# Kernel optimization log

Hardware: AMD Instinct MI355X
Metric: run time of the kernel (lower is better)

Reference implementation:

```python
import jax, jax.numpy as jnp
import numpy as np

N, C, H, W = 512, 256, 14, 14
EPS = 1e-5


def _conv(x, w, pad):
    # x: [N,C,H,W], w: [O,I,kh,kw]
    return jax.lax.conv_general_dilated(
        x, w, window_strides=(1, 1), padding=[(pad, pad), (pad, pad)],
        dimension_numbers=("NCHW", "OIHW", "NCHW"))


def setup_inputs() -> dict:
    key = jax.random.key(0)
    ks = jax.random.split(key, 12)
    x = jax.random.normal(ks[0], (N, C, H, W), jnp.float32)
    gc = jax.random.normal(ks[1], (N, C, H, W), jnp.float32)
    # valid boxes: xmin,ymin in [0,800), w,h in [20,170)
    xy = jax.random.uniform(ks[2], (N, 2), jnp.float32) * 800.0
    wh = jax.random.uniform(ks[3], (N, 2), jnp.float32) * 150.0 + 20.0
    boxes = jnp.concatenate([xy, xy + wh], axis=1)
    classes = jax.random.randint(ks[4], (N,), 0, 2, jnp.int32)
    s3 = 1.0 / np.sqrt(C * 9)
    s1 = 1.0 / np.sqrt(C)
    Wc3 = jax.random.normal(ks[5], (C, C, 3, 3), jnp.float32) * s3
    Wc1 = jax.random.normal(ks[6], (C, C, 1, 1), jnp.float32) * s1
    Wt3 = jax.random.normal(ks[7], (C, C, 3, 3), jnp.float32) * s3
    Wt1 = jax.random.normal(ks[8], (C, C, 1, 1), jnp.float32) * s1
    Wf3 = jax.random.normal(ks[9], (C, C, 3, 3), jnp.float32) * s3
    Wf1 = jax.random.normal(ks[10], (C, C, 1, 1), jnp.float32) * s1
    bn_gamma = jnp.ones((C,), jnp.float32)
    bn_beta = jnp.zeros((C,), jnp.float32)
    bn_mean = jnp.zeros((C,), jnp.float32)
    bn_var = jnp.ones((C,), jnp.float32)
    return dict(x=x, global_context=gc, boxes=boxes, classes=classes,
                Wc3=Wc3, Wc1=Wc1, Wt3=Wt3, Wt1=Wt1, Wf3=Wf3, Wf1=Wf1,
                bn_gamma=bn_gamma, bn_beta=bn_beta, bn_mean=bn_mean, bn_var=bn_var)


def reference(x, global_context, boxes, classes, Wc3, Wc1, Wt3, Wt1, Wf3, Wf1,
              bn_gamma, bn_beta, bn_mean, bn_var):
    # pairwise intersection / self-area gating
    area = (boxes[:, 2] - boxes[:, 0]) * (boxes[:, 3] - boxes[:, 1])  # [N]
    lt = jnp.maximum(boxes[:, None, :2], boxes[None, :, :2])  # [N,N,2]
    rb = jnp.minimum(boxes[:, None, 2:], boxes[None, :, 2:])
    wh = jnp.clip(rb - lt, 0.0)
    inter = wh[..., 0] * wh[..., 1]                            # [N,N]
    inter_percent = inter / area[None, :]                      # divide by area of box j
    mask = (inter_percent > 0.9).astype(x.dtype)               # [N,N]; diag always 1
    counts = mask.sum(axis=1)                                  # [N] >= 1
    # per-instance gather-average of member features
    avg = jnp.einsum("ij,jchw->ichw", mask, x) / counts[:, None, None, None]
    text_in = jnp.where((counts > 1.0)[:, None, None, None], avg, x)
    # branch convs (batched instead of per-proposal loop)
    char_out = _conv(_conv(x, Wc3, 1), Wc1, 0)
    text_out = _conv(_conv(text_in, Wt3, 1), Wt1, 0)
    char_context = jnp.where((classes != 0)[:, None, None, None], char_out, text_out)
    fuse = char_context + x + global_context
    y = _conv(_conv(fuse, Wf3, 1), Wf1, 0)
    inv = jax.lax.rsqrt(bn_var + EPS)
    y = (y - bn_mean[None, :, None, None]) * (bn_gamma * inv)[None, :, None, None] \
        + bn_beta[None, :, None, None]
    return jax.nn.relu(y)
```

## Files before the change

kernel.cpp:

```cpp
#include <hip/hip_runtime.h>

typedef unsigned short u16;
typedef unsigned int u32;
typedef __bf16 bf16x8 __attribute__((ext_vector_type(8)));
typedef float f32x4 __attribute__((ext_vector_type(4)));
typedef u16 u16x4 __attribute__((ext_vector_type(4)));
typedef float f4v __attribute__((ext_vector_type(4)));

#define NB   512
#define CCH  256
#define HW   196
#define LROW 40
#define SSTR 53248

__device__ inline u16 f2bf(float f) {
    u32 u = __float_as_uint(f);
    u32 r = (u + 0x7FFFu + ((u >> 16) & 1u)) >> 16;
    return (u16)r;
}

__global__ void wconv_kernel(const float* __restrict__ Wc3, const float* __restrict__ Wt3,
                             const float* __restrict__ Wf3, const float* __restrict__ Wc1,
                             const float* __restrict__ Wt1, const float* __restrict__ Wf1,
                             u16* __restrict__ w3, u16* __restrict__ w1o)
{
    int bid = blockIdx.x, tid = threadIdx.x;
    if (bid < 768) {
        int wsel = bid >> 8;
        int co = bid & 255;
        const float* src = wsel == 0 ? Wc3 : (wsel == 1 ? Wt3 : Wf3);
#pragma unroll
        for (int rs = 0; rs < 9; ++rs) {
            float v = src[(co * 256 + tid) * 9 + rs];
            w3[wsel * 589824 + (rs * 256 + co) * 256 + tid] = f2bf(v);
        }
    } else {
        int k = (bid - 768) * 256 + tid;
        int wsel = k >> 14;
        int rem = k & 16383;
        const float* src = wsel == 0 ? Wc1 : (wsel == 1 ? Wt1 : Wf1);
        f4v v = *(const f4v*)(src + rem * 4);
        u16x4 o = { f2bf(v.x), f2bf(v.y), f2bf(v.z), f2bf(v.w) };
        *(u16x4*)(w1o + wsel * 65536 + rem * 4) = o;
    }
}

__global__ void mask_kernel(const float* __restrict__ boxes, int* __restrict__ counts,
                            int* __restrict__ members)
{
    int i = blockIdx.x;
    int ln = threadIdx.x;
    __shared__ int cnt;
    if (ln == 0) cnt = 0;
    __syncthreads();
    float xi0 = boxes[i * 4 + 0], yi0 = boxes[i * 4 + 1];
    float xi1 = boxes[i * 4 + 2], yi1 = boxes[i * 4 + 3];
    for (int j = ln; j < NB; j += 64) {
        float xj0 = boxes[j * 4 + 0], yj0 = boxes[j * 4 + 1];
        float xj1 = boxes[j * 4 + 2], yj1 = boxes[j * 4 + 3];
        float areaj = (xj1 - xj0) * (yj1 - yj0);
        float lx = fmaxf(xi0, xj0), ly = fmaxf(yi0, yj0);
        float rx = fminf(xi1, xj1), ry = fminf(yi1, yj1);
        float w = fmaxf(rx - lx, 0.f), h = fmaxf(ry - ly, 0.f);
        if (w * h / areaj > 0.9f) {
            int p = atomicAdd(&cnt, 1);
            members[i * NB + p] = j;
        }
    }
    __syncthreads();
    if (ln == 0) counts[i] = cnt;
}

__global__ void bin_kernel(const float* __restrict__ x, const int* __restrict__ classes,
                           const int* __restrict__ counts, const int* __restrict__ members,
                           u16* __restrict__ bin)
{
    const int s = blockIdx.x, tid = threadIdx.x;
    const int cnt = counts[s];
    u16* binS = bin + s * SSTR;
    if (classes[s] != 0 || cnt <= 1) {
        for (int v = tid; v < 64 * 208; v += 256) {
            int c4 = v / 208;
            int px = v - c4 * 208;
            u16x4 o = {0, 0, 0, 0};
            if (px < HW) {
#pragma unroll
                for (int rg = 0; rg < 4; ++rg)
                    o[rg] = f2bf(x[(s * CCH + c4 * 4 + rg) * HW + px]);
            }
            *(u16x4*)(binS + (c4 * 208 + px) * 4) = o;
        }
    } else {
        __shared__ int mem[NB];
        for (int u = tid; u < cnt; u += 256) mem[u] = members[s * NB + u];
        __syncthreads();
        const float inv = 1.f / (float)cnt;
        for (int v = tid; v < 64 * 208; v += 256) {
            int c4 = v / 208;
            int px = v - c4 * 208;
            u16x4 o = {0, 0, 0, 0};
            if (px < HW) {
                float a[4] = {0.f, 0.f, 0.f, 0.f};
                for (int k = 0; k < cnt; ++k) {
                    const float* xm = x + mem[k] * (CCH * HW);
#pragma unroll
                    for (int rg = 0; rg < 4; ++rg)
                        a[rg] += xm[(c4 * 4 + rg) * HW + px];
                }
#pragma unroll
                for (int rg = 0; rg < 4; ++rg) o[rg] = f2bf(a[rg] * inv);
            }
            *(u16x4*)(binS + (c4 * 208 + px) * 4) = o;
        }
    }
}

__global__ __launch_bounds__(256, 2) void conv3x3_kernel(
    const u16* __restrict__ in, u16* __restrict__ out,
    const u16* __restrict__ w0, const u16* __restrict__ w1,
    const int* __restrict__ classes, int useClass)
{
    __shared__ u16 lds[197 * LROW];
    const int tid = threadIdx.x;
    const int bid = blockIdx.x;
    const int s = bid >> 1;
    const int th = bid & 1;
    const int wv = tid >> 6;
    const int ln = tid & 63;
    const int q = ln >> 4;
    const int l15 = ln & 15;
    const int cobase = wv * 64;
    const int t0 = th * 7;
    const int NT = th ? 6 : 7;

    const u16* wsel = (useClass && classes[s] == 0) ? w1 : w0;

    if (tid < 20) ((u32*)lds)[196 * (LROW / 2) + tid] = 0u;

    int baddr[7], vbits[7];
#pragma unroll
    for (int t = 0; t < 7; ++t) {
        int tt = t0 + t;
        int px = tt * 16 + l15;
        int vb = 0;
        int ba = 196 * LROW + q * 8;
        if (t < NT && px < HW) {
            int y = px / 14;
            int x = px - y * 14;
            ba = px * LROW + q * 8;
#pragma unroll
            for (int rs = 0; rs < 9; ++rs) {
                int iy = y + rs / 3 - 1;
                int ix = x + rs % 3 - 1;
                if (iy >= 0 && iy < 14 && ix >= 0 && ix < 14) vb |= 1 << rs;
            }
        }
        baddr[t] = ba;
        vbits[t] = vb;
    }

    f32x4 acc[4][7];
#pragma unroll
    for (int a = 0; a < 4; ++a)
#pragma unroll
        for (int t = 0; t < 7; ++t) acc[a][t] = (f32x4){0.f, 0.f, 0.f, 0.f};

    const u16* inS = in + s * SSTR;

    for (int cc = 0; cc < 8; ++cc) {
        __syncthreads();
        for (int v = tid; v < 1568; v += 256) {
            int ci4 = v & 7;
            int px = v >> 3;
            u16x4 val = *(const u16x4*)(inS + ((cc * 8 + ci4) * 208 + px) * 4);
            *(u16x4*)(lds + px * LROW + ci4 * 4) = val;
        }
        __syncthreads();

#pragma unroll
        for (int rs = 0; rs < 9; ++rs) {
            const int d = (rs / 3 - 1) * 14 + (rs % 3 - 1);
            bf16x8 af[4];
#pragma unroll
            for (int sub = 0; sub < 4; ++sub)
                af[sub] = *(const bf16x8*)(wsel + ((rs * 256 + cobase + sub * 16 + l15) * 256 + cc * 32 + q * 8));
#pragma unroll
            for (int t = 0; t < 7; ++t) {
                if (t < NT) {
                    int addr = ((vbits[t] >> rs) & 1) ? (baddr[t] + d * LROW)
                                                      : (196 * LROW + q * 8);
                    bf16x8 b = *(const bf16x8*)(lds + addr);
#pragma unroll
                    for (int sub = 0; sub < 4; ++sub)
                        acc[sub][t] = __builtin_amdgcn_mfma_f32_16x16x32_bf16(af[sub], b, acc[sub][t], 0, 0, 0);
                }
            }
        }
    }

#pragma unroll
    for (int sub = 0; sub < 4; ++sub) {
        int co4 = (cobase >> 2) + sub * 4 + q;
#pragma unroll
        for (int t = 0; t < 7; ++t) {
            if (t < NT) {
                int pxs = (t0 + t) * 16 + l15;
                u16x4 o = { f2bf(acc[sub][t][0]), f2bf(acc[sub][t][1]),
                            f2bf(acc[sub][t][2]), f2bf(acc[sub][t][3]) };
                *(u16x4*)(out + (s * (size_t)SSTR) + (co4 * 208 + pxs) * 4) = o;
            }
        }
    }
}

template <int MODE>
__global__ __launch_bounds__(256, 2) void conv1x1_kernel(
    const u16* __restrict__ in, const u16* __restrict__ w0, const u16* __restrict__ w1,
    const int* __restrict__ classes, int useClass,
    const float* __restrict__ xin, const float* __restrict__ gcin,
    const float* __restrict__ gamma, const float* __restrict__ beta,
    const float* __restrict__ mean, const float* __restrict__ var,
    void* __restrict__ outv)
{
    __shared__ u16 lds[197 * LROW];
    const int tid = threadIdx.x;
    const int bid = blockIdx.x;
    const int s = bid >> 1;
    const int th = bid & 1;
    const int wv = tid >> 6;
    const int ln = tid & 63;
    const int q = ln >> 4;
    const int l15 = ln & 15;
    const int cobase = wv * 64;
    const int t0 = th * 7;
    const int NT = th ? 6 : 7;

    const u16* wsel = (useClass && classes[s] == 0) ? w1 : w0;

    if (tid < 20) ((u32*)lds)[196 * (LROW / 2) + tid] = 0u;

    int baddr[7];
#pragma unroll
    for (int t = 0; t < 7; ++t) {
        int px = (t0 + t) * 16 + l15;
        baddr[t] = (t < NT && px < HW ? px : 196) * LROW + q * 8;
    }

    f32x4 acc[4][7];
#pragma unroll
    for (int a = 0; a < 4; ++a)
#pragma unroll
        for (int t = 0; t < 7; ++t) acc[a][t] = (f32x4){0.f, 0.f, 0.f, 0.f};

    const u16* inS = in + s * SSTR;

    for (int cc = 0; cc < 8; ++cc) {
        __syncthreads();
        for (int v = tid; v < 1568; v += 256) {
            int ci4 = v & 7;
            int px = v >> 3;
            u16x4 val = *(const u16x4*)(inS + ((cc * 8 + ci4) * 208 + px) * 4);
            *(u16x4*)(lds + px * LROW + ci4 * 4) = val;
        }
        __syncthreads();

        bf16x8 af[4];
#pragma unroll
        for (int sub = 0; sub < 4; ++sub)
            af[sub] = *(const bf16x8*)(wsel + ((cobase + sub * 16 + l15) * 256 + cc * 32 + q * 8));
#pragma unroll
        for (int t = 0; t < 7; ++t) {
            if (t < NT) {
                bf16x8 b = *(const bf16x8*)(lds + baddr[t]);
#pragma unroll
                for (int sub = 0; sub < 4; ++sub)
                    acc[sub][t] = __builtin_amdgcn_mfma_f32_16x16x32_bf16(af[sub], b, acc[sub][t], 0, 0, 0);
            }
        }
    }

    if (MODE == 0) {
        u16* outb = (u16*)outv;
#pragma unroll
        for (int sub = 0; sub < 4; ++sub) {
            int co4 = (cobase >> 2) + sub * 4 + q;
#pragma unroll
            for (int t = 0; t < 7; ++t) {
                if (t < NT) {
                    int pxs = (t0 + t) * 16 + l15;
                    u16x4 o = {0, 0, 0, 0};
                    if (pxs < HW) {
#pragma unroll
                        for (int rg = 0; rg < 4; ++rg) {
                            int idx = (s * CCH + co4 * 4 + rg) * HW + pxs;
                            o[rg] = f2bf(acc[sub][t][rg] + xin[idx] + gcin[idx]);
                        }
                    }
                    *(u16x4*)(outb + (s * (size_t)SSTR) + (co4 * 208 + pxs) * 4) = o;
                }
            }
        }
    } else {
        float* outf = (float*)outv;
        float scl[4][4], mn[4][4], bt[4][4];
#pragma unroll
        for (int sub = 0; sub < 4; ++sub)
#pragma unroll
            for (int rg = 0; rg < 4; ++rg) {
                int c = cobase + sub * 16 + q * 4 + rg;
                scl[sub][rg] = gamma[c] * rsqrtf(var[c] + 1e-5f);
                mn[sub][rg] = mean[c];
                bt[sub][rg] = beta[c];
            }
#pragma unroll
        for (int sub = 0; sub < 4; ++sub)
#pragma unroll
            for (int t = 0; t < 7; ++t) {
                if (t < NT) {
                    int pxs = (t0 + t) * 16 + l15;
                    if (pxs < HW) {
#pragma unroll
                        for (int rg = 0; rg < 4; ++rg) {
                            int co = cobase + sub * 16 + q * 4 + rg;
                            float v = (acc[sub][t][rg] - mn[sub][rg]) * scl[sub][rg] + bt[sub][rg];
                            outf[(s * CCH + co) * HW + pxs] = fmaxf(v, 0.f);
                        }
                    }
                }
            }
    }
}

extern "C" void kernel_launch(void* const* d_in, const int* in_sizes, int n_in,
                              void* d_out, int out_size, void* d_ws, size_t ws_size,
                              hipStream_t stream)
{
    const float* x    = (const float*)d_in[0];
    const float* gc   = (const float*)d_in[1];
    const float* boxes= (const float*)d_in[2];
    const int*   cls  = (const int*)d_in[3];
    const float* Wc3  = (const float*)d_in[4];
    const float* Wc1  = (const float*)d_in[5];
    const float* Wt3  = (const float*)d_in[6];
    const float* Wt1  = (const float*)d_in[7];
    const float* Wf3  = (const float*)d_in[8];
    const float* Wf1  = (const float*)d_in[9];
    const float* gam  = (const float*)d_in[10];
    const float* bet  = (const float*)d_in[11];
    const float* mea  = (const float*)d_in[12];
    const float* var  = (const float*)d_in[13];
    float* out = (float*)d_out;
    char* ws = (char*)d_ws;

    u16* w3      = (u16*)(ws);
    u16* w1o     = (u16*)(ws + 3538944);
    int* counts  = (int*)(ws + 3932160);
    int* members = (int*)(ws + 3934208);
    u16* bufA    = (u16*)(ws + 4982784);
    u16* bufB    = (u16*)(ws + 59508736);

    wconv_kernel<<<960, 256, 0, stream>>>(Wc3, Wt3, Wf3, Wc1, Wt1, Wf1, w3, w1o);
    mask_kernel<<<512, 64, 0, stream>>>(boxes, counts, members);
    bin_kernel<<<512, 256, 0, stream>>>(x, cls, counts, members, bufA);
    conv3x3_kernel<<<1024, 256, 0, stream>>>(bufA, bufB, w3, w3 + 589824, cls, 1);
    conv1x1_kernel<0><<<1024, 256, 0, stream>>>(bufB, w1o, w1o + 65536, cls, 1, x, gc,
                                                nullptr, nullptr, nullptr, nullptr, (void*)bufA);
    conv3x3_kernel<<<1024, 256, 0, stream>>>(bufA, bufB, w3 + 2 * 589824, w3, cls, 0);
    conv1x1_kernel<1><<<1024, 256, 0, stream>>>(bufB, w1o + 2 * 65536, w1o, cls, 0, nullptr, nullptr,
                                                gam, bet, mea, var, (void*)out);
}
```

Measured before the change: 910.1 us.

## Retile convs by output-channel group and stage 3x3 weights in LDS

Each block now handles one sample and one 64-channel output group instead of half the pixels with all channels. The four waves split the pixel tiles between them and share a single weight slice. For the 3x3 conv, the weights are re-laid out per channel group and chunk, then staged cooperatively into LDS so that all waves reuse them rather than each loading A fragments from global memory. In exchange the activation tile is reloaded four times per sample, LDS use per block grows, and occupancy is raised to 3 blocks per SM.

Result: faster. 872.4 us (-4.1%).

```diff
diff --git a/kernel.cpp b/kernel.cpp
--- a/kernel.cpp
+++ b/kernel.cpp
@@ -5,13 +5,17 @@
 typedef __bf16 bf16x8 __attribute__((ext_vector_type(8)));
 typedef float f32x4 __attribute__((ext_vector_type(4)));
 typedef u16 u16x4 __attribute__((ext_vector_type(4)));
+typedef u16 u16x8 __attribute__((ext_vector_type(8)));
 typedef float f4v __attribute__((ext_vector_type(4)));
 
 #define NB   512
 #define CCH  256
 #define HW   196
 #define LROW 40
+#define ACT_ELEMS (197 * LROW)
+#define WLDS_ELEMS (9 * 64 * 32)
 #define SSTR 53248
+#define CGSTR 147456
 
 __device__ inline u16 f2bf(float f) {
     u32 u = __float_as_uint(f);
@@ -26,13 +30,15 @@
 {
     int bid = blockIdx.x, tid = threadIdx.x;
     if (bid < 768) {
-        int wsel = bid >> 8;
+        int wset = bid >> 8;
         int co = bid & 255;
-        const float* src = wsel == 0 ? Wc3 : (wsel == 1 ? Wt3 : Wf3);
+        int cgi = co >> 6, cop = co & 63;
+        int cc = tid >> 5, cip = tid & 31;
+        const float* src = wset == 0 ? Wc3 : (wset == 1 ? Wt3 : Wf3);
 #pragma unroll
         for (int rs = 0; rs < 9; ++rs) {
             float v = src[(co * 256 + tid) * 9 + rs];
-            w3[wsel * 589824 + (rs * 256 + co) * 256 + tid] = f2bf(v);
+            w3[wset * 589824 + cgi * CGSTR + (cc * 9 + rs) * 2048 + cop * 32 + cip] = f2bf(v);
         }
     } else {
         int k = (bid - 768) * 256 + tid;
@@ -115,33 +121,31 @@
     }
 }
 
-__global__ __launch_bounds__(256, 2) void conv3x3_kernel(
+__global__ __launch_bounds__(256, 3) void conv3x3_kernel(
     const u16* __restrict__ in, u16* __restrict__ out,
     const u16* __restrict__ w0, const u16* __restrict__ w1,
     const int* __restrict__ classes, int useClass)
 {
-    __shared__ u16 lds[197 * LROW];
+    __shared__ u16 lds[ACT_ELEMS + WLDS_ELEMS];
     const int tid = threadIdx.x;
     const int bid = blockIdx.x;
-    const int s = bid >> 1;
-    const int th = bid & 1;
+    const int s  = bid >> 2;
+    const int cg = bid & 3;
     const int wv = tid >> 6;
     const int ln = tid & 63;
     const int q = ln >> 4;
     const int l15 = ln & 15;
-    const int cobase = wv * 64;
-    const int t0 = th * 7;
-    const int NT = th ? 6 : 7;
-
-    const u16* wsel = (useClass && classes[s] == 0) ? w1 : w0;
+    const int t0 = (wv == 0) ? 0 : (wv == 1 ? 4 : (wv == 2 ? 7 : 10));
+    const int NT = (wv == 0) ? 4 : 3;
+
+    const u16* wsel = (((useClass && classes[s] == 0) ? w1 : w0)) + cg * CGSTR;
 
     if (tid < 20) ((u32*)lds)[196 * (LROW / 2) + tid] = 0u;
 
-    int baddr[7], vbits[7];
-#pragma unroll
-    for (int t = 0; t < 7; ++t) {
-        int tt = t0 + t;
-        int px = tt * 16 + l15;
+    int baddr[4], vbits[4];
+#pragma unroll
+    for (int t = 0; t < 4; ++t) {
+        int px = (t0 + t) * 16 + l15;
         int vb = 0;
         int ba = 196 * LROW + q * 8;
         if (t < NT && px < HW) {
@@ -159,11 +163,11 @@
         vbits[t] = vb;
     }
 
-    f32x4 acc[4][7];
+    f32x4 acc[4][4];
 #pragma unroll
     for (int a = 0; a < 4; ++a)
 #pragma unroll
-        for (int t = 0; t < 7; ++t) acc[a][t] = (f32x4){0.f, 0.f, 0.f, 0.f};
+        for (int t = 0; t < 4; ++t) acc[a][t] = (f32x4){0.f, 0.f, 0.f, 0.f};
 
     const u16* inS = in + s * SSTR;
 
@@ -175,6 +179,14 @@
             u16x4 val = *(const u16x4*)(inS + ((cc * 8 + ci4) * 208 + px) * 4);
             *(u16x4*)(lds + px * LROW + ci4 * 4) = val;
         }
+        {
+            const u16* wcc = wsel + cc * WLDS_ELEMS;
+#pragma unroll
+            for (int k = 0; k < 9; ++k) {
+                int idx = tid + k * 256;
+                *(u16x8*)(lds + ACT_ELEMS + idx * 8) = *(const u16x8*)(wcc + idx * 8);
+            }
+        }
         __syncthreads();
 
 #pragma unroll
@@ -183,9 +195,9 @@
             bf16x8 af[4];
 #pragma unroll
             for (int sub = 0; sub < 4; ++sub)
-                af[sub] = *(const bf16x8*)(wsel + ((rs * 256 + cobase + sub * 16 + l15) * 256 + cc * 32 + q * 8));
-#pragma unroll
-            for (int t = 0; t < 7; ++t) {
+                af[sub] = *(const bf16x8*)(lds + ACT_ELEMS + rs * 2048 + (sub * 16 + l15) * 32 + q * 8);
+#pragma unroll
+            for (int t = 0; t < 4; ++t) {
                 if (t < NT) {
                     int addr = ((vbits[t] >> rs) & 1) ? (baddr[t] + d * LROW)
                                                       : (196 * LROW + q * 8);
@@ -200,9 +212,9 @@
 
 #pragma unroll
     for (int sub = 0; sub < 4; ++sub) {
-        int co4 = (cobase >> 2) + sub * 4 + q;
-#pragma unroll
-        for (int t = 0; t < 7; ++t) {
+        int co4 = cg * 16 + sub * 4 + q;
+#pragma unroll
+        for (int t = 0; t < 4; ++t) {
             if (t < NT) {
                 int pxs = (t0 + t) * 16 + l15;
                 u16x4 o = { f2bf(acc[sub][t][0]), f2bf(acc[sub][t][1]),
@@ -214,7 +226,7 @@
 }
 
 template <int MODE>
-__global__ __launch_bounds__(256, 2) void conv1x1_kernel(
+__global__ __launch_bounds__(256, 3) void conv1x1_kernel(
     const u16* __restrict__ in, const u16* __restrict__ w0, const u16* __restrict__ w1,
     const int* __restrict__ classes, int useClass,
     const float* __restrict__ xin, const float* __restrict__ gcin,
@@ -222,35 +234,34 @@
     const float* __restrict__ mean, const float* __restrict__ var,
     void* __restrict__ outv)
 {
-    __shared__ u16 lds[197 * LROW];
+    __shared__ u16 lds[ACT_ELEMS];
     const int tid = threadIdx.x;
     const int bid = blockIdx.x;
-    const int s = bid >> 1;
-    const int th = bid & 1;
+    const int s  = bid >> 2;
+    const int cg = bid & 3;
     const int wv = tid >> 6;
     const int ln = tid & 63;
     const int q = ln >> 4;
     const int l15 = ln & 15;
-    const int cobase = wv * 64;
-    const int t0 = th * 7;
-    const int NT = th ? 6 : 7;
+    const int t0 = (wv == 0) ? 0 : (wv == 1 ? 4 : (wv == 2 ? 7 : 10));
+    const int NT = (wv == 0) ? 4 : 3;
 
     const u16* wsel = (useClass && classes[s] == 0) ? w1 : w0;
 
     if (tid < 20) ((u32*)lds)[196 * (LROW / 2) + tid] = 0u;
 
-    int baddr[7];
-#pragma unroll
-    for (int t = 0; t < 7; ++t) {
+    int baddr[4];
+#pragma unroll
+    for (int t = 0; t < 4; ++t) {
         int px = (t0 + t) * 16 + l15;
         baddr[t] = (t < NT && px < HW ? px : 196) * LROW + q * 8;
     }
 
-    f32x4 acc[4][7];
+    f32x4 acc[4][4];
 #pragma unroll
     for (int a = 0; a < 4; ++a)
 #pragma unroll
-        for (int t = 0; t < 7; ++t) acc[a][t] = (f32x4){0.f, 0.f, 0.f, 0.f};
+        for (int t = 0; t < 4; ++t) acc[a][t] = (f32x4){0.f, 0.f, 0.f, 0.f};
 
     const u16* inS = in + s * SSTR;
 
@@ -267,9 +278,9 @@
         bf16x8 af[4];
 #pragma unroll
         for (int sub = 0; sub < 4; ++sub)
-            af[sub] = *(const bf16x8*)(wsel + ((cobase + sub * 16 + l15) * 256 + cc * 32 + q * 8));
-#pragma unroll
-        for (int t = 0; t < 7; ++t) {
+            af[sub] = *(const bf16x8*)(wsel + ((cg * 64 + sub * 16 + l15) * 256 + cc * 32 + q * 8));
+#pragma unroll
+        for (int t = 0; t < 4; ++t) {
             if (t < NT) {
                 bf16x8 b = *(const bf16x8*)(lds + baddr[t]);
 #pragma unroll
@@ -283,9 +294,9 @@
         u16* outb = (u16*)outv;
 #pragma unroll
         for (int sub = 0; sub < 4; ++sub) {
-            int co4 = (cobase >> 2) + sub * 4 + q;
-#pragma unroll
-            for (int t = 0; t < 7; ++t) {
+            int co4 = cg * 16 + sub * 4 + q;
+#pragma unroll
+            for (int t = 0; t < 4; ++t) {
                 if (t < NT) {
                     int pxs = (t0 + t) * 16 + l15;
                     u16x4 o = {0, 0, 0, 0};
@@ -307,7 +318,7 @@
         for (int sub = 0; sub < 4; ++sub)
 #pragma unroll
             for (int rg = 0; rg < 4; ++rg) {
-                int c = cobase + sub * 16 + q * 4 + rg;
+                int c = cg * 64 + sub * 16 + q * 4 + rg;
                 scl[sub][rg] = gamma[c] * rsqrtf(var[c] + 1e-5f);
                 mn[sub][rg] = mean[c];
                 bt[sub][rg] = beta[c];
@@ -315,13 +326,13 @@
 #pragma unroll
         for (int sub = 0; sub < 4; ++sub)
 #pragma unroll
-            for (int t = 0; t < 7; ++t) {
+            for (int t = 0; t < 4; ++t) {
                 if (t < NT) {
                     int pxs = (t0 + t) * 16 + l15;
                     if (pxs < HW) {
 #pragma unroll
                         for (int rg = 0; rg < 4; ++rg) {
-                            int co = cobase + sub * 16 + q * 4 + rg;
+                            int co = cg * 64 + sub * 16 + q * 4 + rg;
                             float v = (acc[sub][t][rg] - mn[sub][rg]) * scl[sub][rg] + bt[sub][rg];
                             outf[(s * CCH + co) * HW + pxs] = fmaxf(v, 0.f);
                         }
@@ -362,10 +373,10 @@
     wconv_kernel<<<960, 256, 0, stream>>>(Wc3, Wt3, Wf3, Wc1, Wt1, Wf1, w3, w1o);
     mask_kernel<<<512, 64, 0, stream>>>(boxes, counts, members);
     bin_kernel<<<512, 256, 0, stream>>>(x, cls, counts, members, bufA);
-    conv3x3_kernel<<<1024, 256, 0, stream>>>(bufA, bufB, w3, w3 + 589824, cls, 1);
-    conv1x1_kernel<0><<<1024, 256, 0, stream>>>(bufB, w1o, w1o + 65536, cls, 1, x, gc,
+    conv3x3_kernel<<<2048, 256, 0, stream>>>(bufA, bufB, w3, w3 + 589824, cls, 1);
+    conv1x1_kernel<0><<<2048, 256, 0, stream>>>(bufB, w1o, w1o + 65536, cls, 1, x, gc,
                                                 nullptr, nullptr, nullptr, nullptr, (void*)bufA);
-    conv3x3_kernel<<<1024, 256, 0, stream>>>(bufA, bufB, w3 + 2 * 589824, w3, cls, 0);
-    conv1x1_kernel<1><<<1024, 256, 0, stream>>>(bufB, w1o + 2 * 65536, w1o, cls, 0, nullptr, nullptr,
+    conv3x3_kernel<<<2048, 256, 0, stream>>>(bufA, bufB, w3 + 2 * 589824, w3, cls, 0);
+    conv1x1_kernel<1><<<2048, 256, 0, stream>>>(bufB, w1o + 2 * 65536, w1o, cls, 0, nullptr, nullptr,
                                                 gam, bet, mea, var, (void*)out);
 }
```
